# Kernel tuning notes

Measured on AMD Instinct MI355X. Metric: run time of the kernel, lower is better.

## Reference

```python
import jax, jax.numpy as jnp
import numpy as np

N_NODES = 50000
N_EDGES = 800000
HID = 64


def fake_quant_w(w):
    # symmetric per-tensor int8 fake quantization (num_bits=8)
    s = jnp.maximum(jnp.max(jnp.abs(w)) / 127.0, 1e-8)
    q = jnp.clip(jnp.round(w / s), -127.0, 127.0) * s
    return w + jax.lax.stop_gradient(q - w)


def layer_norm(x, g, b, eps=1e-5):
    mu = jnp.mean(x, axis=-1, keepdims=True)
    var = jnp.var(x, axis=-1, keepdims=True)
    return (x - mu) * jax.lax.rsqrt(var + eps) * g + b


def pointnet_conv(x, pos, src, dst, W, n_nodes):
    # message: cat([x_j, pos_j - pos_i]) @ W_q^T, max-aggregated at i (dst)
    rel = pos[src] - pos[dst]                       # [E, 3]
    feat = jnp.concatenate([x[src], rel], axis=-1)  # [E, C+3]
    msg = feat @ fake_quant_w(W).T                  # [E, 64]
    h = jax.ops.segment_max(msg, dst, num_segments=n_nodes)
    return jnp.where(jnp.isfinite(h), h, 0.0)       # empty segments -> 0


def setup_inputs() -> dict:
    key = jax.random.key(0)
    ks = jax.random.split(key, 16)
    d = {}
    d["x"] = jax.random.normal(ks[0], (N_NODES, 1), jnp.float32)
    d["pos"] = jax.random.normal(ks[1], (N_NODES, 3), jnp.float32)
    d["edge_index"] = jax.random.randint(ks[2], (2, N_EDGES), 0, N_NODES, jnp.int32)
    sc = 0.02
    d["W0"] = jax.random.normal(ks[3], (HID, 1 + 3), jnp.float32) * sc
    d["Ws"] = jax.random.normal(ks[4], (4, HID, HID + 3), jnp.float32) * sc
    d["ln_g"] = jnp.ones((5, HID), jnp.float32)
    d["ln_b"] = jnp.zeros((5, HID), jnp.float32)
    d["mlp_w1"] = jax.random.normal(ks[5], (128, 320), jnp.float32) * sc
    d["mlp_b1"] = jnp.zeros((128,), jnp.float32)
    d["mlp_w2"] = jax.random.normal(ks[6], (128, 128), jnp.float32) * sc
    d["mlp_b2"] = jnp.zeros((128,), jnp.float32)
    d["mlp_w3"] = jax.random.normal(ks[7], (64, 128), jnp.float32) * sc
    d["mlp_b3"] = jnp.zeros((64,), jnp.float32)
    d["mlp_w4"] = jax.random.normal(ks[8], (2, 64), jnp.float32) * sc
    d["mlp_b4"] = jnp.zeros((2,), jnp.float32)
    d["scale"] = jnp.ones((2,), jnp.float32)
    return d


def reference(x, pos, edge_index, W0, Ws, ln_g, ln_b,
              mlp_w1, mlp_b1, mlp_w2, mlp_b2, mlp_w3, mlp_b3, mlp_w4, mlp_b4,
              scale):
    src, dst = edge_index[0], edge_index[1]
    n = x.shape[0]
    embeddings = []
    h = x
    for i in range(5):
        W = W0 if i == 0 else Ws[i - 1]
        h = pointnet_conv(h, pos, src, dst, W, n)
        h = layer_norm(h, ln_g[i], ln_b[i])
        h = jax.nn.relu(h)
        embeddings.append(h)
    z = jnp.concatenate(embeddings, axis=-1)  # [N, 320]
    z = layer_norm(z, jnp.ones((z.shape[-1],), z.dtype), jnp.zeros((z.shape[-1],), z.dtype))
    z = jax.nn.relu(z @ mlp_w1.T + mlp_b1)
    z = jax.nn.relu(z @ mlp_w2.T + mlp_b2)
    z = jax.nn.relu(z @ mlp_w3.T + mlp_b3)
    flow = (z @ mlp_w4.T + mlp_b4) * scale
    return flow
```

## Files before the change

### kernel.cpp

```cpp
#include <hip/hip_runtime.h>
#include <hip/hip_bf16.h>

#define N_NODES 50000
#define N_EDGES 800000
#define NBLK 196

__device__ __forceinline__ float bf2f(unsigned short u) {
    union { unsigned int i; float f; } c; c.i = ((unsigned int)u) << 16; return c.f;
}
__device__ __forceinline__ unsigned short f2bf(float f) {
    union { float f; unsigned int u; } c; c.f = f;
    unsigned int u = c.u;
    u += 0x7fffu + ((u >> 16) & 1u);
    return (unsigned short)(u >> 16);
}
__device__ __forceinline__ float ldin(const void* p, long i, int f32) {
    return f32 ? ((const float*)p)[i] : bf2f(((const unsigned short*)p)[i]);
}
__device__ __forceinline__ float wsum(float v) {
#pragma unroll
    for (int m = 32; m; m >>= 1) v += __shfl_xor(v, m, 64);
    return v;
}

__global__ void probe_kernel(const unsigned short* __restrict__ lng, int* __restrict__ flag) {
    if (threadIdx.x == 0 && blockIdx.x == 0)
        flag[0] = (lng[0] == 0x3F80 && lng[1] == 0x3F80) ? 0 : 1;
}

__global__ __launch_bounds__(256) void hist_kernel(const int* __restrict__ ei, int* __restrict__ deg) {
    int e = blockIdx.x * 256 + threadIdx.x;
    if (e < N_EDGES) atomicAdd(&deg[ei[N_EDGES + e]], 1);
}

__global__ __launch_bounds__(256) void bsum_kernel(const int* __restrict__ deg,
                                                   int* __restrict__ bsum) {
    __shared__ int wt[4];
    const int t = threadIdx.x, lane = t & 63, wid = t >> 6;
    const int i = blockIdx.x * 256 + t;
    int v = (i < N_NODES) ? deg[i] : 0;
    int r = v;
#pragma unroll
    for (int m = 32; m; m >>= 1) r += __shfl_xor(r, m, 64);
    if (lane == 0) wt[wid] = r;
    __syncthreads();
    if (t == 0) bsum[blockIdx.x] = wt[0] + wt[1] + wt[2] + wt[3];
}

__global__ __launch_bounds__(256) void boff_kernel(const int* __restrict__ bsum,
                                                   int* __restrict__ boff) {
    __shared__ int wt[4];
    const int t = threadIdx.x, lane = t & 63, wid = t >> 6;
    int v = (t < NBLK) ? bsum[t] : 0;
    int inc = v;
#pragma unroll
    for (int off = 1; off < 64; off <<= 1) {
        int u = __shfl_up(inc, off, 64);
        if (lane >= off) inc += u;
    }
    if (lane == 63) wt[wid] = inc;
    __syncthreads();
    int woff = 0;
    for (int w = 0; w < wid; ++w) woff += wt[w];
    if (t < NBLK) boff[t] = inc - v + woff;
}

__global__ __launch_bounds__(256) void scanout_kernel(const int* __restrict__ deg,
                                                      const int* __restrict__ boff,
                                                      int* __restrict__ rowptr,
                                                      int* __restrict__ cursor) {
    __shared__ int wt[4];
    const int t = threadIdx.x, lane = t & 63, wid = t >> 6;
    const int i = blockIdx.x * 256 + t;
    int v = (i < N_NODES) ? deg[i] : 0;
    int inc = v;
#pragma unroll
    for (int off = 1; off < 64; off <<= 1) {
        int u = __shfl_up(inc, off, 64);
        if (lane >= off) inc += u;
    }
    if (lane == 63) wt[wid] = inc;
    __syncthreads();
    int woff = 0;
    for (int w = 0; w < wid; ++w) woff += wt[w];
    int excl = inc - v + woff + boff[blockIdx.x];
    if (i < N_NODES) {
        rowptr[i] = excl;
        cursor[i] = excl;
        if (i == N_NODES - 1) rowptr[N_NODES] = excl + v;
    }
}

__global__ __launch_bounds__(256) void scatter_kernel(const int* __restrict__ ei,
                                                      int* __restrict__ cursor,
                                                      int* __restrict__ csr_src) {
    int e = blockIdx.x * 256 + threadIdx.x;
    if (e < N_EDGES) {
        int src = ei[e];
        int dst = ei[N_EDGES + e];
        int p = atomicAdd(&cursor[dst], 1);
        csr_src[p] = src;
    }
}

__global__ __launch_bounds__(256) void quant_kernel(const void* __restrict__ W0,
                                                    const void* __restrict__ Ws,
                                                    float* __restrict__ Wc0,
                                                    float* __restrict__ Wc,
                                                    float* __restrict__ Wr,
                                                    const int* __restrict__ flagp) {
    const int f32 = *flagp;
    int layer = blockIdx.x;
    const void* src = (layer == 0) ? W0 : Ws;
    long sbase = (layer == 0) ? 0 : (long)(layer - 1) * 4288;
    float* dstc = (layer == 0) ? Wc0 : Wc + (size_t)(layer - 1) * 4352;
    float* dstr = (layer == 0) ? nullptr : Wr + (size_t)(layer - 1) * 4352;
    int Ki = (layer == 0) ? 4 : 67;
    int n = 64 * Ki;
    __shared__ float red[256];
    float amax = 0.0f;
    for (int i = threadIdx.x; i < n; i += 256) amax = fmaxf(amax, fabsf(ldin(src, sbase + i, f32)));
    red[threadIdx.x] = amax;
    __syncthreads();
    for (int s = 128; s > 0; s >>= 1) {
        if (threadIdx.x < s) red[threadIdx.x] = fmaxf(red[threadIdx.x], red[threadIdx.x + s]);
        __syncthreads();
    }
    float sc = fmaxf(red[0] / 127.0f, 1e-8f);
    for (int i = threadIdx.x; i < n; i += 256) {
        float w = ldin(src, sbase + i, f32);
        float q = rintf(w / sc);
        q = fminf(fmaxf(q, -127.0f), 127.0f);
        float v = q * sc;
        int o = i / Ki, k = i % Ki;
        dstc[(size_t)k * 64 + o] = v;
        if (dstr) dstr[(size_t)o * 68 + k] = v;
    }
}

__global__ __launch_bounds__(256) void wcvt_kernel(const void* __restrict__ w1,
                                                   const void* __restrict__ w2,
                                                   const void* __restrict__ w3,
                                                   float* __restrict__ Wm,
                                                   const int* __restrict__ flagp) {
    const int f32 = *flagp;
    const int i = blockIdx.x * 256 + threadIdx.x;
    if (i < 40960) Wm[i] = ldin(w1, i, f32);
    else if (i < 57344) Wm[i] = ldin(w2, i - 40960, f32);
    else if (i < 65536) Wm[i] = ldin(w3, i - 57344, f32);
}

__global__ __launch_bounds__(256) void u0_kernel(const void* __restrict__ x,
                                                 const void* __restrict__ pos,
                                                 const float* __restrict__ Wc0,
                                                 float* __restrict__ u,
                                                 const int* __restrict__ flagp) {
    const int f32 = *flagp;
    const int n = blockIdx.x * 256 + threadIdx.x;
    if (n >= N_NODES) return;
    const float xv = ldin(x, n, f32);
    const float p0 = ldin(pos, 3L * n + 0, f32);
    const float p1 = ldin(pos, 3L * n + 1, f32);
    const float p2 = ldin(pos, 3L * n + 2, f32);
    float4* up = reinterpret_cast<float4*>(u + (size_t)n * 64);
#pragma unroll
    for (int q = 0; q < 16; ++q) {
        const float4 w0 = *reinterpret_cast<const float4*>(Wc0 + 0 * 64 + 4 * q);
        const float4 w1 = *reinterpret_cast<const float4*>(Wc0 + 1 * 64 + 4 * q);
        const float4 w2 = *reinterpret_cast<const float4*>(Wc0 + 2 * 64 + 4 * q);
        const float4 w3 = *reinterpret_cast<const float4*>(Wc0 + 3 * 64 + 4 * q);
        float4 o;
        o.x = fmaf(p2, w3.x, fmaf(p1, w2.x, fmaf(p0, w1.x, xv * w0.x)));
        o.y = fmaf(p2, w3.y, fmaf(p1, w2.y, fmaf(p0, w1.y, xv * w0.y)));
        o.z = fmaf(p2, w3.z, fmaf(p1, w2.z, fmaf(p0, w1.z, xv * w0.z)));
        o.w = fmaf(p2, w3.w, fmaf(p1, w2.w, fmaf(p0, w1.w, xv * w0.w)));
        up[q] = o;
    }
}

__global__ __launch_bounds__(256) void agg_kernel(const float* __restrict__ u,
                                                  const void* __restrict__ pos,
                                                  const int* __restrict__ rowptr,
                                                  const int* __restrict__ csr,
                                                  const float* __restrict__ WcV, int vrow,
                                                  const void* __restrict__ lng,
                                                  const void* __restrict__ lnb,
                                                  int lnoff,
                                                  float* __restrict__ z, int out_off,
                                                  float2* __restrict__ stats,
                                                  const int* __restrict__ flagp) {
    const int f32 = *flagp;
    const int lane = threadIdx.x & 63;
    const int n = __builtin_amdgcn_readfirstlane((blockIdx.x * 256 + threadIdx.x) >> 6);
    if (n >= N_NODES) return;
    const int e0 = rowptr[n], e1 = rowptr[n + 1];
    float acc = -INFINITY;
    int e = e0;
    for (; e + 16 <= e1; e += 16) {
        float t0 = u[(size_t)csr[e + 0] * 64 + lane];
        float t1 = u[(size_t)csr[e + 1] * 64 + lane];
        float t2 = u[(size_t)csr[e + 2] * 64 + lane];
        float t3 = u[(size_t)csr[e + 3] * 64 + lane];
        float t4 = u[(size_t)csr[e + 4] * 64 + lane];
        float t5 = u[(size_t)csr[e + 5] * 64 + lane];
        float t6 = u[(size_t)csr[e + 6] * 64 + lane];
        float t7 = u[(size_t)csr[e + 7] * 64 + lane];
        float t8 = u[(size_t)csr[e + 8] * 64 + lane];
        float t9 = u[(size_t)csr[e + 9] * 64 + lane];
        float ta = u[(size_t)csr[e + 10] * 64 + lane];
        float tb = u[(size_t)csr[e + 11] * 64 + lane];
        float tc = u[(size_t)csr[e + 12] * 64 + lane];
        float td = u[(size_t)csr[e + 13] * 64 + lane];
        float te = u[(size_t)csr[e + 14] * 64 + lane];
        float tf = u[(size_t)csr[e + 15] * 64 + lane];
        float m0 = fmaxf(fmaxf(t0, t1), fmaxf(t2, t3));
        float m1 = fmaxf(fmaxf(t4, t5), fmaxf(t6, t7));
        float m2 = fmaxf(fmaxf(t8, t9), fmaxf(ta, tb));
        float m3 = fmaxf(fmaxf(tc, td), fmaxf(te, tf));
        acc = fmaxf(acc, fmaxf(fmaxf(m0, m1), fmaxf(m2, m3)));
    }
    for (; e + 4 <= e1; e += 4) {
        float t0 = u[(size_t)csr[e + 0] * 64 + lane];
        float t1 = u[(size_t)csr[e + 1] * 64 + lane];
        float t2 = u[(size_t)csr[e + 2] * 64 + lane];
        float t3 = u[(size_t)csr[e + 3] * 64 + lane];
        acc = fmaxf(acc, fmaxf(fmaxf(t0, t1), fmaxf(t2, t3)));
    }
    for (; e < e1; ++e)
        acc = fmaxf(acc, u[(size_t)csr[e] * 64 + lane]);
    const float p0 = ldin(pos, 3L * n + 0, f32);
    const float p1 = ldin(pos, 3L * n + 1, f32);
    const float p2 = ldin(pos, 3L * n + 2, f32);
    const float v = fmaf(p2, WcV[(size_t)(vrow + 2) * 64 + lane],
                    fmaf(p1, WcV[(size_t)(vrow + 1) * 64 + lane],
                         p0 * WcV[(size_t)(vrow + 0) * 64 + lane]));
    float h = acc - v;
    if (!isfinite(h)) h = 0.0f;
    const float g = ldin(lng, lnoff + lane, f32);
    const float bb = ldin(lnb, lnoff + lane, f32);
    const float mu = wsum(h) * (1.0f / 64.0f);
    const float dd = h - mu;
    const float var = wsum(dd * dd) * (1.0f / 64.0f);
    float y = dd * rsqrtf(var + 1e-5f) * g + bb;
    y = fmaxf(y, 0.0f);
    z[(size_t)n * 320 + out_off + lane] = y;
    if (stats) {
        const float* zr = z + (size_t)n * 320;
        const float v0 = zr[0 * 64 + lane];
        const float v1 = zr[1 * 64 + lane];
        const float v2 = zr[2 * 64 + lane];
        const float v3 = zr[3 * 64 + lane];
        const float s = ((v0 + v1) + (v2 + v3)) + y;
        const float mu2 = wsum(s) * (1.0f / 320.0f);
        float q = (v0 - mu2) * (v0 - mu2);
        q = fmaf(v1 - mu2, v1 - mu2, q);
        q = fmaf(v2 - mu2, v2 - mu2, q);
        q = fmaf(v3 - mu2, v3 - mu2, q);
        q = fmaf(y - mu2, y - mu2, q);
        const float var2 = wsum(q) * (1.0f / 320.0f);
        if (lane == 0) stats[n] = make_float2(mu2, rsqrtf(var2 + 1e-5f));
    }
}

__global__ __launch_bounds__(256) void un_kernel(const float* __restrict__ z, int in_off,
                                                 const float* __restrict__ Wr,
                                                 const void* __restrict__ pos,
                                                 float* __restrict__ un,
                                                 const int* __restrict__ flagp) {
    __shared__ float At[16][68];
    __shared__ float Wt[16][68];
    const int f32 = *flagp;
    const int tid = threadIdx.x;
    const int bn = blockIdx.x * 64;
    const int o_base = (tid & 15) * 4;
    const int n_base = (tid >> 4) * 4;
    const int sr = tid >> 2;
    const int kq = (tid & 3) * 4;
    float acc[4][4] = {};
    float4 av = make_float4(0.f, 0.f, 0.f, 0.f);
    if (bn + sr < N_NODES)
        av = *reinterpret_cast<const float4*>(z + (size_t)(bn + sr) * 320 + in_off + kq);
    float4 wv = *reinterpret_cast<const float4*>(Wr + (size_t)sr * 68 + kq);
    for (int kk = 0; kk < 64; kk += 16) {
        __syncthreads();
        At[kq + 0][sr] = av.x; At[kq + 1][sr] = av.y; At[kq + 2][sr] = av.z; At[kq + 3][sr] = av.w;
        Wt[kq + 0][sr] = wv.x; Wt[kq + 1][sr] = wv.y; Wt[kq + 2][sr] = wv.z; Wt[kq + 3][sr] = wv.w;
        __syncthreads();
        if (kk + 16 < 64) {
            av = make_float4(0.f, 0.f, 0.f, 0.f);
            if (bn + sr < N_NODES)
                av = *reinterpret_cast<const float4*>(z + (size_t)(bn + sr) * 320 + in_off + kk + 16 + kq);
            wv = *reinterpret_cast<const float4*>(Wr + (size_t)sr * 68 + kk + 16 + kq);
        }
#pragma unroll
        for (int k = 0; k < 16; ++k) {
            const float4 a4 = *reinterpret_cast<const float4*>(&At[k][n_base]);
            const float4 w4 = *reinterpret_cast<const float4*>(&Wt[k][o_base]);
            const float a[4] = { a4.x, a4.y, a4.z, a4.w };
            const float ww[4] = { w4.x, w4.y, w4.z, w4.w };
#pragma unroll
            for (int i = 0; i < 4; ++i)
#pragma unroll
                for (int j = 0; j < 4; ++j)
                    acc[i][j] = fmaf(a[i], ww[j], acc[i][j]);
        }
    }
    float wp[3][4];
#pragma unroll
    for (int c = 0; c < 3; ++c)
#pragma unroll
        for (int j = 0; j < 4; ++j)
            wp[c][j] = Wr[(size_t)(o_base + j) * 68 + 64 + c];
#pragma unroll
    for (int i = 0; i < 4; ++i) {
        const int n = bn + n_base + i;
        if (n < N_NODES) {
            const float p0 = ldin(pos, 3L * n + 0, f32);
            const float p1 = ldin(pos, 3L * n + 1, f32);
            const float p2 = ldin(pos, 3L * n + 2, f32);
#pragma unroll
            for (int j = 0; j < 4; ++j)
                un[(size_t)n * 64 + o_base + j] =
                    fmaf(p2, wp[2][j], fmaf(p1, wp[1][j], fmaf(p0, wp[0][j], acc[i][j])));
        }
    }
}

__global__ __launch_bounds__(256) void gemm128_kernel(const float* __restrict__ A,
                                                      const float* __restrict__ W,
                                                      const void* __restrict__ bias,
                                                      const float2* __restrict__ stats,
                                                      float* __restrict__ C,
                                                      int Ki,
                                                      const int* __restrict__ flagp) {
    __shared__ float At[16][68];
    __shared__ float Wt[16][132];
    const int f32 = *flagp;
    const int tid = threadIdx.x;
    const int bn = blockIdx.x * 64;
    const int sr = tid >> 2;
    const int kq = (tid & 3) * 4;
    const int wr = tid >> 1;
    const int kq2 = (tid & 1) * 8;
    const int n_base = (tid >> 4) * 4;
    const int o_base = (tid & 15) * 8;
    float mu = 0.f, rs = 1.f;
    if (stats && bn + sr < N_NODES) { float2 st = stats[bn + sr]; mu = st.x; rs = st.y; }
    float acc[4][8] = {};
    float4 av = make_float4(0.f, 0.f, 0.f, 0.f);
    if (bn + sr < N_NODES)
        av = *reinterpret_cast<const float4*>(A + (size_t)(bn + sr) * Ki + kq);
    float4 wv0 = *reinterpret_cast<const float4*>(W + (size_t)wr * Ki + kq2);
    float4 wv1 = *reinterpret_cast<const float4*>(W + (size_t)wr * Ki + kq2 + 4);
    for (int kk = 0; kk < Ki; kk += 16) {
        __syncthreads();
        At[kq + 0][sr] = (av.x - mu) * rs;
        At[kq + 1][sr] = (av.y - mu) * rs;
        At[kq + 2][sr] = (av.z - mu) * rs;
        At[kq + 3][sr] = (av.w - mu) * rs;
        Wt[kq2 + 0][wr] = wv0.x; Wt[kq2 + 1][wr] = wv0.y;
        Wt[kq2 + 2][wr] = wv0.z; Wt[kq2 + 3][wr] = wv0.w;
        Wt[kq2 + 4][wr] = wv1.x; Wt[kq2 + 5][wr] = wv1.y;
        Wt[kq2 + 6][wr] = wv1.z; Wt[kq2 + 7][wr] = wv1.w;
        __syncthreads();
        if (kk + 16 < Ki) {
            av = make_float4(0.f, 0.f, 0.f, 0.f);
            if (bn + sr < N_NODES)
                av = *reinterpret_cast<const float4*>(A + (size_t)(bn + sr) * Ki + kk + 16 + kq);
            wv0 = *reinterpret_cast<const float4*>(W + (size_t)wr * Ki + kk + 16 + kq2);
            wv1 = *reinterpret_cast<const float4*>(W + (size_t)wr * Ki + kk + 16 + kq2 + 4);
        }
#pragma unroll
        for (int k = 0; k < 16; ++k) {
            const float4 a4 = *reinterpret_cast<const float4*>(&At[k][n_base]);
            const float4 wa = *reinterpret_cast<const float4*>(&Wt[k][o_base]);
            const float4 wb = *reinterpret_cast<const float4*>(&Wt[k][o_base + 4]);
            const float a[4] = { a4.x, a4.y, a4.z, a4.w };
            const float ww[8] = { wa.x, wa.y, wa.z, wa.w, wb.x, wb.y, wb.z, wb.w };
#pragma unroll
            for (int i = 0; i < 4; ++i)
#pragma unroll
                for (int j = 0; j < 8; ++j)
                    acc[i][j] = fmaf(a[i], ww[j], acc[i][j]);
        }
    }
    float bj[8];
#pragma unroll
    for (int j = 0; j < 8; ++j) bj[j] = ldin(bias, o_base + j, f32);
#pragma unroll
    for (int i = 0; i < 4; ++i) {
        const int n = bn + n_base + i;
        if (n < N_NODES) {
            float4 c0, c1;
            c0.x = fmaxf(acc[i][0] + bj[0], 0.f); c0.y = fmaxf(acc[i][1] + bj[1], 0.f);
            c0.z = fmaxf(acc[i][2] + bj[2], 0.f); c0.w = fmaxf(acc[i][3] + bj[3], 0.f);
            c1.x = fmaxf(acc[i][4] + bj[4], 0.f); c1.y = fmaxf(acc[i][5] + bj[5], 0.f);
            c1.z = fmaxf(acc[i][6] + bj[6], 0.f); c1.w = fmaxf(acc[i][7] + bj[7], 0.f);
            *reinterpret_cast<float4*>(C + (size_t)n * 128 + o_base) = c0;
            *reinterpret_cast<float4*>(C + (size_t)n * 128 + o_base + 4) = c1;
        }
    }
}

__global__ __launch_bounds__(256) void gemm64out_kernel(const float* __restrict__ A,
                                                        const float* __restrict__ W,
                                                        const void* __restrict__ bias,
                                                        const void* __restrict__ w4,
                                                        const void* __restrict__ b4,
                                                        const void* __restrict__ scale,
                                                        void* __restrict__ out,
                                                        const int* __restrict__ flagp) {
    __shared__ float At[16][68];
    __shared__ float Wt[16][68];
    __shared__ float h3t[64][65];
    const int f32 = *flagp;
    const int tid = threadIdx.x;
    const int bn = blockIdx.x * 64;
    const int Ki = 128;
    const int o_base = (tid & 15) * 4;
    const int n_base = (tid >> 4) * 4;
    const int sr = tid >> 2;
    const int kq = (tid & 3) * 4;
    float acc[4][4] = {};
    float4 av = make_float4(0.f, 0.f, 0.f, 0.f);
    if (bn + sr < N_NODES)
        av = *reinterpret_cast<const float4*>(A + (size_t)(bn + sr) * Ki + kq);
    float4 wv = *reinterpret_cast<const float4*>(W + (size_t)sr * Ki + kq);
    for (int kk = 0; kk < Ki; kk += 16) {
        __syncthreads();
        At[kq + 0][sr] = av.x; At[kq + 1][sr] = av.y; At[kq + 2][sr] = av.z; At[kq + 3][sr] = av.w;
        Wt[kq + 0][sr] = wv.x; Wt[kq + 1][sr] = wv.y; Wt[kq + 2][sr] = wv.z; Wt[kq + 3][sr] = wv.w;
        __syncthreads();
        if (kk + 16 < Ki) {
            av = make_float4(0.f, 0.f, 0.f, 0.f);
            if (bn + sr < N_NODES)
                av = *reinterpret_cast<const float4*>(A + (size_t)(bn + sr) * Ki + kk + 16 + kq);
            wv = *reinterpret_cast<const float4*>(W + (size_t)sr * Ki + kk + 16 + kq);
        }
#pragma unroll
        for (int k = 0; k < 16; ++k) {
            const float4 a4 = *reinterpret_cast<const float4*>(&At[k][n_base]);
            const float4 w4v = *reinterpret_cast<const float4*>(&Wt[k][o_base]);
            const float a[4] = { a4.x, a4.y, a4.z, a4.w };
            const float ww[4] = { w4v.x, w4v.y, w4v.z, w4v.w };
#pragma unroll
            for (int i = 0; i < 4; ++i)
#pragma unroll
                for (int j = 0; j < 4; ++j)
                    acc[i][j] = fmaf(a[i], ww[j], acc[i][j]);
        }
    }
    float bj[4];
#pragma unroll
    for (int j = 0; j < 4; ++j) bj[j] = ldin(bias, o_base + j, f32);
    __syncthreads();
#pragma unroll
    for (int i = 0; i < 4; ++i)
#pragma unroll
        for (int j = 0; j < 4; ++j)
            h3t[n_base + i][o_base + j] = fmaxf(acc[i][j] + bj[j], 0.f);
    __syncthreads();
    const int lane = tid & 63, wid = tid >> 6;
    const float wa = ldin(w4, lane, f32);
    const float wb = ldin(w4, 64 + lane, f32);
    const float b0 = ldin(b4, 0, f32), b1 = ldin(b4, 1, f32);
    const float s0 = ldin(scale, 0, f32), s1 = ldin(scale, 1, f32);
#pragma unroll
    for (int r = wid * 16; r < wid * 16 + 16; ++r) {
        const int n = bn + r;
        if (n >= N_NODES) break;
        const float hv = h3t[r][lane];
        const float d0 = wsum(hv * wa);
        const float d1 = wsum(hv * wb);
        if (lane == 0) {
            const float o0 = (d0 + b0) * s0;
            const float o1 = (d1 + b1) * s1;
            if (f32) {
                ((float*)out)[n * 2 + 0] = o0;
                ((float*)out)[n * 2 + 1] = o1;
            } else {
                ((unsigned short*)out)[n * 2 + 0] = f2bf(o0);
                ((unsigned short*)out)[n * 2 + 1] = f2bf(o1);
            }
        }
    }
}

extern "C" void kernel_launch(void* const* d_in, const int* in_sizes, int n_in,
                              void* d_out, int out_size, void* d_ws, size_t ws_size,
                              hipStream_t stream) {
    (void)in_sizes; (void)n_in; (void)out_size; (void)ws_size;
    const void* x    = d_in[0];
    const void* pos  = d_in[1];
    const int*  ei   = (const int*)d_in[2];
    const void* W0   = d_in[3];
    const void* Ws   = d_in[4];
    const void* lng  = d_in[5];
    const void* lnb  = d_in[6];
    const void* w1   = d_in[7];
    const void* b1   = d_in[8];
    const void* w2   = d_in[9];
    const void* b2   = d_in[10];
    const void* w3   = d_in[11];
    const void* b3   = d_in[12];
    const void* w4   = d_in[13];
    const void* b4   = d_in[14];
    const void* scl  = d_in[15];

    float* z      = (float*)d_ws;
    float* h1     = z + 16000000;
    float* Wc0    = h1 + 6400000;
    float* Wc     = Wc0 + 256;
    float* Wr     = Wc + 17408;
    float* Wm     = Wr + 17408;
    int*   deg    = (int*)(Wm + 65536);
    int*   rowptr = deg + N_NODES;
    int*   cursor = rowptr + (N_NODES + 1);
    int*   flag   = cursor + N_NODES;
    int*   csr    = flag + 1;
    int*   bsum   = csr + N_EDGES;
    int*   boff   = bsum + 256;
    float2* stats = (float2*)(boff + 256);
    float* Wm1 = Wm, *Wm2 = Wm + 40960, *Wm3 = Wm + 57344;
    float* ua     = h1;
    float* ub     = h1 + 3200000;
    float* h2 = z;

    hipMemsetAsync(deg, 0, N_NODES * sizeof(int), stream);
    probe_kernel<<<1, 64, 0, stream>>>((const unsigned short*)lng, flag);
    hist_kernel<<<(N_EDGES + 255) / 256, 256, 0, stream>>>(ei, deg);
    bsum_kernel<<<NBLK, 256, 0, stream>>>(deg, bsum);
    boff_kernel<<<1, 256, 0, stream>>>(bsum, boff);
    scanout_kernel<<<NBLK, 256, 0, stream>>>(deg, boff, rowptr, cursor);
    scatter_kernel<<<(N_EDGES + 255) / 256, 256, 0, stream>>>(ei, cursor, csr);
    quant_kernel<<<5, 256, 0, stream>>>(W0, Ws, Wc0, Wc, Wr, flag);
    wcvt_kernel<<<256, 256, 0, stream>>>(w1, w2, w3, Wm, flag);

    const int gagg = (N_NODES * 64 + 255) / 256;
    const int gun  = (N_NODES + 63) / 64;

    u0_kernel<<<NBLK, 256, 0, stream>>>(x, pos, Wc0, ua, flag);
    agg_kernel<<<gagg, 256, 0, stream>>>(ua, pos, rowptr, csr, Wc0, 1,
                                         lng, lnb, 0, z, 0, nullptr, flag);
    un_kernel<<<gun, 256, 0, stream>>>(z, 0, Wr + 0 * 4352, pos, ub, flag);
    agg_kernel<<<gagg, 256, 0, stream>>>(ub, pos, rowptr, csr, Wc + 0 * 4352, 64,
                                         lng, lnb, 64, z, 64, nullptr, flag);
    un_kernel<<<gun, 256, 0, stream>>>(z, 64, Wr + 1 * 4352, pos, ua, flag);
    agg_kernel<<<gagg, 256, 0, stream>>>(ua, pos, rowptr, csr, Wc + 1 * 4352, 64,
                                         lng, lnb, 128, z, 128, nullptr, flag);
    un_kernel<<<gun, 256, 0, stream>>>(z, 128, Wr + 2 * 4352, pos, ub, flag);
    agg_kernel<<<gagg, 256, 0, stream>>>(ub, pos, rowptr, csr, Wc + 2 * 4352, 64,
                                         lng, lnb, 192, z, 192, nullptr, flag);
    un_kernel<<<gun, 256, 0, stream>>>(z, 192, Wr + 3 * 4352, pos, ua, flag);
    agg_kernel<<<gagg, 256, 0, stream>>>(ua, pos, rowptr, csr, Wc + 3 * 4352, 64,
                                         lng, lnb, 256, z, 256, stats, flag);

    const int gg = (N_NODES + 63) / 64;
    gemm128_kernel<<<gg, 256, 0, stream>>>(z, Wm1, b1, stats, h1, 320, flag);
    gemm128_kernel<<<gg, 256, 0, stream>>>(h1, Wm2, b2, nullptr, h2, 128, flag);
    gemm64out_kernel<<<gg, 256, 0, stream>>>(h2, Wm3, b3, w4, b4, scl, d_out, flag);
}
```

Before: 571.3 us.

## Drop probe kernel, merge weight prep kernels, split MLP GEMMs over output halves

Removes the dtype probe kernel and has every kernel derive the input dtype directly from the layer-norm gain values. The weight quantization and MLP weight conversion kernels are merged into one launch. The 128-wide MLP GEMMs are replaced with a 64x64-tile kernel launched over a 2D grid that splits the output columns, which doubles the block count and lowers per-thread register use, at the cost of reading the A tile twice. Each fewer launch also removes one step of launch overhead.

After: 588.7 us. +3.0%, slower.

```diff
diff --git a/kernel.cpp b/kernel.cpp
--- a/kernel.cpp
+++ b/kernel.cpp
@@ -14,6 +14,10 @@
     u += 0x7fffu + ((u >> 16) & 1u);
     return (unsigned short)(u >> 16);
 }
+__device__ __forceinline__ int is_f32(const void* lng) {
+    const unsigned short* p = (const unsigned short*)lng;
+    return !(p[0] == 0x3F80 && p[1] == 0x3F80);
+}
 __device__ __forceinline__ float ldin(const void* p, long i, int f32) {
     return f32 ? ((const float*)p)[i] : bf2f(((const unsigned short*)p)[i]);
 }
@@ -21,11 +25,6 @@
 #pragma unroll
     for (int m = 32; m; m >>= 1) v += __shfl_xor(v, m, 64);
     return v;
-}
-
-__global__ void probe_kernel(const unsigned short* __restrict__ lng, int* __restrict__ flag) {
-    if (threadIdx.x == 0 && blockIdx.x == 0)
-        flag[0] = (lng[0] == 0x3F80 && lng[1] == 0x3F80) ? 0 : 1;
 }
 
 __global__ __launch_bounds__(256) void hist_kernel(const int* __restrict__ ei, int* __restrict__ deg) {
@@ -103,13 +102,24 @@
     }
 }
 
-__global__ __launch_bounds__(256) void quant_kernel(const void* __restrict__ W0,
-                                                    const void* __restrict__ Ws,
-                                                    float* __restrict__ Wc0,
-                                                    float* __restrict__ Wc,
-                                                    float* __restrict__ Wr,
-                                                    const int* __restrict__ flagp) {
-    const int f32 = *flagp;
+__global__ __launch_bounds__(256) void prep_kernel(const void* __restrict__ W0,
+                                                   const void* __restrict__ Ws,
+                                                   const void* __restrict__ w1,
+                                                   const void* __restrict__ w2,
+                                                   const void* __restrict__ w3,
+                                                   float* __restrict__ Wc0,
+                                                   float* __restrict__ Wc,
+                                                   float* __restrict__ Wr,
+                                                   float* __restrict__ Wm,
+                                                   const void* __restrict__ lng) {
+    const int f32 = is_f32(lng);
+    if (blockIdx.x >= 5) {
+        const int i = (blockIdx.x - 5) * 256 + threadIdx.x;
+        if (i < 40960) Wm[i] = ldin(w1, i, f32);
+        else if (i < 57344) Wm[i] = ldin(w2, i - 40960, f32);
+        else if (i < 65536) Wm[i] = ldin(w3, i - 57344, f32);
+        return;
+    }
     int layer = blockIdx.x;
     const void* src = (layer == 0) ? W0 : Ws;
     long sbase = (layer == 0) ? 0 : (long)(layer - 1) * 4288;
@@ -138,24 +148,12 @@
     }
 }
 
-__global__ __launch_bounds__(256) void wcvt_kernel(const void* __restrict__ w1,
-                                                   const void* __restrict__ w2,
-                                                   const void* __restrict__ w3,
-                                                   float* __restrict__ Wm,
-                                                   const int* __restrict__ flagp) {
-    const int f32 = *flagp;
-    const int i = blockIdx.x * 256 + threadIdx.x;
-    if (i < 40960) Wm[i] = ldin(w1, i, f32);
-    else if (i < 57344) Wm[i] = ldin(w2, i - 40960, f32);
-    else if (i < 65536) Wm[i] = ldin(w3, i - 57344, f32);
-}
-
 __global__ __launch_bounds__(256) void u0_kernel(const void* __restrict__ x,
                                                  const void* __restrict__ pos,
                                                  const float* __restrict__ Wc0,
                                                  float* __restrict__ u,
-                                                 const int* __restrict__ flagp) {
-    const int f32 = *flagp;
+                                                 const void* __restrict__ lng) {
+    const int f32 = is_f32(lng);
     const int n = blockIdx.x * 256 + threadIdx.x;
     if (n >= N_NODES) return;
     const float xv = ldin(x, n, f32);
@@ -187,9 +185,8 @@
                                                   const void* __restrict__ lnb,
                                                   int lnoff,
                                                   float* __restrict__ z, int out_off,
-                                                  float2* __restrict__ stats,
-                                                  const int* __restrict__ flagp) {
-    const int f32 = *flagp;
+                                                  float2* __restrict__ stats) {
+    const int f32 = is_f32(lng);
     const int lane = threadIdx.x & 63;
     const int n = __builtin_amdgcn_readfirstlane((blockIdx.x * 256 + threadIdx.x) >> 6);
     if (n >= N_NODES) return;
@@ -266,10 +263,10 @@
                                                  const float* __restrict__ Wr,
                                                  const void* __restrict__ pos,
                                                  float* __restrict__ un,
-                                                 const int* __restrict__ flagp) {
+                                                 const void* __restrict__ lng) {
     __shared__ float At[16][68];
     __shared__ float Wt[16][68];
-    const int f32 = *flagp;
+    const int f32 = is_f32(lng);
     const int tid = threadIdx.x;
     const int bn = blockIdx.x * 64;
     const int o_base = (tid & 15) * 4;
@@ -326,78 +323,70 @@
     }
 }
 
-__global__ __launch_bounds__(256) void gemm128_kernel(const float* __restrict__ A,
-                                                      const float* __restrict__ W,
-                                                      const void* __restrict__ bias,
-                                                      const float2* __restrict__ stats,
-                                                      float* __restrict__ C,
-                                                      int Ki,
-                                                      const int* __restrict__ flagp) {
+__global__ __launch_bounds__(256) void gemm64_kernel(const float* __restrict__ A,
+                                                     const float* __restrict__ W,
+                                                     const void* __restrict__ bias,
+                                                     const float2* __restrict__ stats,
+                                                     float* __restrict__ C,
+                                                     int Ki, int Ko,
+                                                     const void* __restrict__ lng) {
     __shared__ float At[16][68];
-    __shared__ float Wt[16][132];
-    const int f32 = *flagp;
+    __shared__ float Wt[16][68];
+    const int f32 = is_f32(lng);
     const int tid = threadIdx.x;
     const int bn = blockIdx.x * 64;
+    const int bo = blockIdx.y * 64;
+    const int o_base = (tid & 15) * 4;
+    const int n_base = (tid >> 4) * 4;
     const int sr = tid >> 2;
     const int kq = (tid & 3) * 4;
-    const int wr = tid >> 1;
-    const int kq2 = (tid & 1) * 8;
-    const int n_base = (tid >> 4) * 4;
-    const int o_base = (tid & 15) * 8;
     float mu = 0.f, rs = 1.f;
     if (stats && bn + sr < N_NODES) { float2 st = stats[bn + sr]; mu = st.x; rs = st.y; }
-    float acc[4][8] = {};
+    float acc[4][4] = {};
     float4 av = make_float4(0.f, 0.f, 0.f, 0.f);
     if (bn + sr < N_NODES)
         av = *reinterpret_cast<const float4*>(A + (size_t)(bn + sr) * Ki + kq);
-    float4 wv0 = *reinterpret_cast<const float4*>(W + (size_t)wr * Ki + kq2);
-    float4 wv1 = *reinterpret_cast<const float4*>(W + (size_t)wr * Ki + kq2 + 4);
+    float4 wv = *reinterpret_cast<const float4*>(W + (size_t)(bo + sr) * Ki + kq);
     for (int kk = 0; kk < Ki; kk += 16) {
         __syncthreads();
         At[kq + 0][sr] = (av.x - mu) * rs;
         At[kq + 1][sr] = (av.y - mu) * rs;
         At[kq + 2][sr] = (av.z - mu) * rs;
         At[kq + 3][sr] = (av.w - mu) * rs;
-        Wt[kq2 + 0][wr] = wv0.x; Wt[kq2 + 1][wr] = wv0.y;
-        Wt[kq2 + 2][wr] = wv0.z; Wt[kq2 + 3][wr] = wv0.w;
-        Wt[kq2 + 4][wr] = wv1.x; Wt[kq2 + 5][wr] = wv1.y;
-        Wt[kq2 + 6][wr] = wv1.z; Wt[kq2 + 7][wr] = wv1.w;
+        Wt[kq + 0][sr] = wv.x; Wt[kq + 1][sr] = wv.y; Wt[kq + 2][sr] = wv.z; Wt[kq + 3][sr] = wv.w;
         __syncthreads();
         if (kk + 16 < Ki) {
             av = make_float4(0.f, 0.f, 0.f, 0.f);
             if (bn + sr < N_NODES)
                 av = *reinterpret_cast<const float4*>(A + (size_t)(bn + sr) * Ki + kk + 16 + kq);
-            wv0 = *reinterpret_cast<const float4*>(W + (size_t)wr * Ki + kk + 16 + kq2);
-            wv1 = *reinterpret_cast<const float4*>(W + (size_t)wr * Ki + kk + 16 + kq2 + 4);
+            wv = *reinterpret_cast<const float4*>(W + (size_t)(bo + sr) * Ki + kk + 16 + kq);
         }
 #pragma unroll
         for (int k = 0; k < 16; ++k) {
             const float4 a4 = *reinterpret_cast<const float4*>(&At[k][n_base]);
-            const float4 wa = *reinterpret_cast<const float4*>(&Wt[k][o_base]);
-            const float4 wb = *reinterpret_cast<const float4*>(&Wt[k][o_base + 4]);
+            const float4 w4 = *reinterpret_cast<const float4*>(&Wt[k][o_base]);
             const float a[4] = { a4.x, a4.y, a4.z, a4.w };
-            const float ww[8] = { wa.x, wa.y, wa.z, wa.w, wb.x, wb.y, wb.z, wb.w };
+            const float ww[4] = { w4.x, w4.y, w4.z, w4.w };
 #pragma unroll
             for (int i = 0; i < 4; ++i)
 #pragma unroll
-                for (int j = 0; j < 8; ++j)
+                for (int j = 0; j < 4; ++j)
                     acc[i][j] = fmaf(a[i], ww[j], acc[i][j]);
         }
     }
-    float bj[8];
-#pragma unroll
-    for (int j = 0; j < 8; ++j) bj[j] = ldin(bias, o_base + j, f32);
+    float bj[4];
+#pragma unroll
+    for (int j = 0; j < 4; ++j) bj[j] = ldin(bias, bo + o_base + j, f32);
 #pragma unroll
     for (int i = 0; i < 4; ++i) {
         const int n = bn + n_base + i;
         if (n < N_NODES) {
-            float4 c0, c1;
-            c0.x = fmaxf(acc[i][0] + bj[0], 0.f); c0.y = fmaxf(acc[i][1] + bj[1], 0.f);
-            c0.z = fmaxf(acc[i][2] + bj[2], 0.f); c0.w = fmaxf(acc[i][3] + bj[3], 0.f);
-            c1.x = fmaxf(acc[i][4] + bj[4], 0.f); c1.y = fmaxf(acc[i][5] + bj[5], 0.f);
-            c1.z = fmaxf(acc[i][6] + bj[6], 0.f); c1.w = fmaxf(acc[i][7] + bj[7], 0.f);
-            *reinterpret_cast<float4*>(C + (size_t)n * 128 + o_base) = c0;
-            *reinterpret_cast<float4*>(C + (size_t)n * 128 + o_base + 4) = c1;
+            float4 c0;
+            c0.x = fmaxf(acc[i][0] + bj[0], 0.f);
+            c0.y = fmaxf(acc[i][1] + bj[1], 0.f);
+            c0.z = fmaxf(acc[i][2] + bj[2], 0.f);
+            c0.w = fmaxf(acc[i][3] + bj[3], 0.f);
+            *reinterpret_cast<float4*>(C + (size_t)n * Ko + bo + o_base) = c0;
         }
     }
 }
@@ -409,11 +398,11 @@
                                                         const void* __restrict__ b4,
                                                         const void* __restrict__ scale,
                                                         void* __restrict__ out,
-                                                        const int* __restrict__ flagp) {
+                                                        const void* __restrict__ lng) {
     __shared__ float At[16][68];
     __shared__ float Wt[16][68];
     __shared__ float h3t[64][65];
-    const int f32 = *flagp;
+    const int f32 = is_f32(lng);
     const int tid = threadIdx.x;
     const int bn = blockIdx.x * 64;
     const int Ki = 128;
@@ -508,55 +497,54 @@
     const void* scl  = d_in[15];
 
     float* z      = (float*)d_ws;
-    float* h1     = z + 16000000;
-    float* Wc0    = h1 + 6400000;
+    float* ua     = z + 16000000;
+    float* ub     = ua + 3200000;
+    float* Wc0    = ub + 3200000;
     float* Wc     = Wc0 + 256;
     float* Wr     = Wc + 17408;
     float* Wm     = Wr + 17408;
     int*   deg    = (int*)(Wm + 65536);
     int*   rowptr = deg + N_NODES;
     int*   cursor = rowptr + (N_NODES + 1);
-    int*   flag   = cursor + N_NODES;
-    int*   csr    = flag + 1;
+    int*   csr    = cursor + N_NODES;
     int*   bsum   = csr + N_EDGES;
     int*   boff   = bsum + 256;
     float2* stats = (float2*)(boff + 256);
     float* Wm1 = Wm, *Wm2 = Wm + 40960, *Wm3 = Wm + 57344;
-    float* ua     = h1;
-    float* ub     = h1 + 3200000;
+    float* h1 = ua;
     float* h2 = z;
 
     hipMemsetAsync(deg, 0, N_NODES * sizeof(int), stream);
-    probe_kernel<<<1, 64, 0, stream>>>((const unsigned short*)lng, flag);
     hist_kernel<<<(N_EDGES + 255) / 256, 256, 0, stream>>>(ei, deg);
     bsum_kernel<<<NBLK, 256, 0, stream>>>(deg, bsum);
     boff_kernel<<<1, 256, 0, stream>>>(bsum, boff);
     scanout_kernel<<<NBLK, 256, 0, stream>>>(deg, boff, rowptr, cursor);
     scatter_kernel<<<(N_EDGES + 255) / 256, 256, 0, stream>>>(ei, cursor, csr);
-    quant_kernel<<<5, 256, 0, stream>>>(W0, Ws, Wc0, Wc, Wr, flag);
-    wcvt_kernel<<<256, 256, 0, stream>>>(w1, w2, w3, Wm, flag);
+    prep_kernel<<<261, 256, 0, stream>>>(W0, Ws, w1, w2, w3, Wc0, Wc, Wr, Wm, lng);
 
     const int gagg = (N_NODES * 64 + 255) / 256;
     const int gun  = (N_NODES + 63) / 64;
 
-    u0_kernel<<<NBLK, 256, 0, stream>>>(x, pos, Wc0, ua, flag);
+    u0_kernel<<<NBLK, 256, 0, stream>>>(x, pos, Wc0, ua, lng);
     agg_kernel<<<gagg, 256, 0, stream>>>(ua, pos, rowptr, csr, Wc0, 1,
-                                         lng, lnb, 0, z, 0, nullptr, flag);
-    un_kernel<<<gun, 256, 0, stream>>>(z, 0, Wr + 0 * 4352, pos, ub, flag);
+                                         lng, lnb, 0, z, 0, nullptr);
+    un_kernel<<<gun, 256, 0, stream>>>(z, 0, Wr + 0 * 4352, pos, ub, lng);
     agg_kernel<<<gagg, 256, 0, stream>>>(ub, pos, rowptr, csr, Wc + 0 * 4352, 64,
-                                         lng, lnb, 64, z, 64, nullptr, flag);
-    un_kernel<<<gun, 256, 0, stream>>>(z, 64, Wr + 1 * 4352, pos, ua, flag);
+                                         lng, lnb, 64, z, 64, nullptr);
+    un_kernel<<<gun, 256, 0, stream>>>(z, 64, Wr + 1 * 4352, pos, ua, lng);
     agg_kernel<<<gagg, 256, 0, stream>>>(ua, pos, rowptr, csr, Wc + 1 * 4352, 64,
-                                         lng, lnb, 128, z, 128, nullptr, flag);
-    un_kernel<<<gun, 256, 0, stream>>>(z, 128, Wr + 2 * 4352, pos, ub, flag);
+                                         lng, lnb, 128, z, 128, nullptr);
+    un_kernel<<<gun, 256, 0, stream>>>(z, 128, Wr + 2 * 4352, pos, ub, lng);
     agg_kernel<<<gagg, 256, 0, stream>>>(ub, pos, rowptr, csr, Wc + 2 * 4352, 64,
-                                         lng, lnb, 192, z, 192, nullptr, flag);
-    un_kernel<<<gun, 256, 0, stream>>>(z, 192, Wr + 3 * 4352, pos, ua, flag);
+                                         lng, lnb, 192, z, 192, nullptr);
+    un_kernel<<<gun, 256, 0, stream>>>(z, 192, Wr + 3 * 4352, pos, ua, lng);
     agg_kernel<<<gagg, 256, 0, stream>>>(ua, pos, rowptr, csr, Wc + 3 * 4352, 64,
-                                         lng, lnb, 256, z, 256, stats, flag);
+                                         lng, lnb, 256, z, 256, stats);
 
     const int gg = (N_NODES + 63) / 64;
-    gemm128_kernel<<<gg, 256, 0, stream>>>(z, Wm1, b1, stats, h1, 320, flag);
-    gemm128_kernel<<<gg, 256, 0, stream>>>(h1, Wm2, b2, nullptr, h2, 128, flag);
-    gemm64out_kernel<<<gg, 256, 0, stream>>>(h2, Wm3, b3, w4, b4, scl, d_out, flag);
-}
+    dim3 g1(gg, 2);
+    gemm64_kernel<<<g1, 256, 0, stream>>>(z, Wm1, b1, stats, h1, 320, 128, lng);
+    dim3 g2(gg, 2);
+    gemm64_kernel<<<g2, 256, 0, stream>>>(h1, Wm2, b2, nullptr, h2, 128, 128, lng);
+    gemm64out_kernel<<<gg, 256, 0, stream>>>(h2, Wm3, b3, w4, b4, scl, d_out, lng);
+}
```
